# Kernel optimization log

Measured on AMD Instinct MI355X. Metric: run time of the kernel, lower is better.

The kernel has to match this reference:

```python
import jax, jax.numpy as jnp
import numpy as np

EPS = 1e-8


def setup_inputs() -> dict:
    key = jax.random.key(0)
    k1, k2, k3, k4 = jax.random.split(key, 4)
    b, cin, cout, H, W, ksz = 8, 512, 512, 64, 64, 3
    return {
        "x": jax.random.normal(k1, (b, cin, H, W), dtype=jnp.float32),
        "style": jax.random.normal(k2, (b, cin), dtype=jnp.float32),
        "noise": jax.random.normal(k3, (b, 1, H, W), dtype=jnp.float32),
        "weight": jax.random.normal(k4, (cout, cin, ksz, ksz), dtype=jnp.float32),
        "bias": jnp.zeros((1, cout, 1, 1), dtype=jnp.float32),
        "noise_strength": jnp.zeros((), dtype=jnp.float32),
    }


def reference(x, style, noise, weight, bias, noise_strength):
    cout, cin, k, _ = weight.shape
    b, _, H, W = x.shape
    scale = (1.0 / (cin * k * k)) ** 0.5

    # weight scaled and normalized by per-filter inf-norm
    w = weight * scale / jnp.max(jnp.abs(weight), axis=(1, 2, 3), keepdims=True)
    # style normalized by per-sample inf-norm
    s = style / jnp.max(jnp.abs(style), axis=1, keepdims=True)

    # modulate: (b, cout, cin, k, k)
    w = w[None] * s[:, None, :, None, None]
    # demodulate
    demod = jnp.sqrt(jnp.sum(w * w, axis=(2, 3, 4)) + EPS)  # (b, cout)
    w = w / demod[:, :, None, None, None]

    # grouped conv: one group per sample (note: input is scaled again, as in source)
    xr = (x * scale).reshape(1, b * cin, H, W)
    wr = w.reshape(b * cout, cin, k, k)
    out = jax.lax.conv_general_dilated(
        xr, wr, window_strides=(1, 1), padding=((1, 1), (1, 1)),
        dimension_numbers=("NCHW", "OIHW", "NCHW"), feature_group_count=b)
    out = out.reshape(b, cout, H, W) + bias
    out = out + noise * noise_strength
    return out
```

## Files before the change

kernel.cpp:

```cpp
#include <hip/hip_runtime.h>


#define EPSV   1e-8f
#define SCALEV 0.014731391274719738f

typedef __attribute__((ext_vector_type(8))) short short8;
typedef __attribute__((ext_vector_type(4))) float floatx4;

__device__ __forceinline__ void gload_lds16(const void* g, void* l) {
    __builtin_amdgcn_global_load_lds(
        (const __attribute__((address_space(1))) void*)g,
        (__attribute__((address_space(3))) void*)l, 16, 0, 0);
}

__device__ __forceinline__ unsigned short f2bf(float f) {
    unsigned u = __float_as_uint(f);
    unsigned r = (u + 0x7fffu + ((u >> 16) & 1u)) >> 16;
    return (unsigned short)r;
}

__global__ __launch_bounds__(256) void zero_border(uint4* __restrict__ xbp4) {
    int idx = blockIdx.x * 256 + threadIdx.x;
    if (idx >= 133120) return;
    int q    = idx & 63;
    int cell = (idx >> 6) % 260;
    int b    = idx / 16640;
    int h, w;
    if (cell < 66)       { h = 0;  w = cell; }
    else if (cell < 132) { h = 65; w = cell - 66; }
    else { int e = cell - 132; h = 1 + (e >> 1); w = (e & 1) * 65; }
    uint4 z = {0u, 0u, 0u, 0u};
    xbp4[(size_t)((b * 66 + h) * 66 + w) * 64 + q] = z;
}

__global__ __launch_bounds__(512) void prep_style(
    const float* __restrict__ style, float* __restrict__ tbuf)
{
    const int b = blockIdx.x, t = threadIdx.x;
    float v = style[b * 512 + t];
    __shared__ float red[512];
    red[t] = fabsf(v);
    __syncthreads();
    for (int s = 256; s > 0; s >>= 1) {
        if (t < s) red[t] = fmaxf(red[t], red[t + s]);
        __syncthreads();
    }
    tbuf[b * 512 + t] = v / red[0];
}

__global__ __launch_bounds__(256) void prep_w(
    const float* __restrict__ weight, float* __restrict__ wsqn,
    unsigned short* __restrict__ Aw)
{
    const int co = blockIdx.x, t = threadIdx.x;
    const float* wp = weight + (size_t)co * 4608;
    float m = 0.f;
    for (int i = t; i < 4608; i += 256) m = fmaxf(m, fabsf(wp[i]));
    __shared__ float red[256];
    red[t] = m;
    __syncthreads();
    for (int s = 128; s > 0; s >>= 1) {
        if (t < s) red[t] = fmaxf(red[t], red[t + s]);
        __syncthreads();
    }
    const float inv = 1.f / red[0];
    for (int ci = t; ci < 512; ci += 256) {
        float s = 0.f;
        #pragma unroll
        for (int k = 0; k < 9; ++k) {
            float v = wp[ci * 9 + k] * inv;
            s = fmaf(v, v, s);
            Aw[(size_t)(co * 9 + k) * 512 + ci] = f2bf(v);
        }
        wsqn[co * 512 + ci] = s;
    }
}

__global__ __launch_bounds__(256) void prep_x(
    const float* __restrict__ x, const float* __restrict__ tbuf,
    unsigned short* __restrict__ xbp)
{
    const int cic = blockIdx.x;
    const int h   = blockIdx.y;
    const int b   = blockIdx.z;
    const int tid = threadIdx.x;
    __shared__ float tr[64][33];

    const int cl = tid >> 3;
    const int w0 = (tid & 7) << 3;
    const int ci = cic * 32 + cl;
    const float tv = tbuf[b * 512 + ci];
    const float* xp = x + (((size_t)(b * 512 + ci)) << 12) + (h << 6) + w0;
    float4 u = *(const float4*)xp;
    float4 v = *(const float4*)(xp + 4);
    tr[w0 + 0][cl] = u.x * tv; tr[w0 + 1][cl] = u.y * tv;
    tr[w0 + 2][cl] = u.z * tv; tr[w0 + 3][cl] = u.w * tv;
    tr[w0 + 4][cl] = v.x * tv; tr[w0 + 5][cl] = v.y * tv;
    tr[w0 + 6][cl] = v.z * tv; tr[w0 + 7][cl] = v.w * tv;
    __syncthreads();

    const int w  = tid >> 2;
    const int c8 = (tid & 3) << 3;
    unsigned short o[8] __attribute__((aligned(16)));
    #pragma unroll
    for (int j = 0; j < 8; ++j) o[j] = f2bf(tr[w][c8 + j]);
    size_t dst = ((size_t)((b * 66 + h + 1) * 66) + (w + 1)) * 512 + cic * 32 + c8;
    *(uint4*)&xbp[dst] = *(const uint4*)o;
}

__global__ __launch_bounds__(256) void gcoef(
    const float* __restrict__ wsqn, const float* __restrict__ tbuf,
    float* __restrict__ gbuf)
{
    const int b    = blockIdx.y;
    const int co   = blockIdx.x * 4 + (threadIdx.x >> 6);
    const int lane = threadIdx.x & 63;
    float sum = 0.f;
    for (int ci = lane; ci < 512; ci += 64) {
        float tv = tbuf[b * 512 + ci];
        sum = fmaf(tv * tv, wsqn[co * 512 + ci], sum);
    }
    #pragma unroll
    for (int off = 32; off > 0; off >>= 1) sum += __shfl_down(sum, off);
    if (lane == 0)
        gbuf[b * 512 + co] = SCALEV * SCALEV / sqrtf(fmaf(SCALEV * SCALEV, sum, EPSV));
}

__global__ __launch_bounds__(256, 2) void conv_mfma(
    const unsigned short* __restrict__ xbp, const unsigned short* __restrict__ Aw,
    const float* __restrict__ gbuf, const float* __restrict__ bias,
    const float* __restrict__ noise, const float* __restrict__ nstr,
    float* __restrict__ out)
{
    __shared__ __align__(16) short sA[2][8192];
    __shared__ __align__(16) short sB[2][6656];

    const int tid  = threadIdx.x;
    const int lane = tid & 63;
    const int wv   = tid >> 6;
    const int b    = blockIdx.z;
    const int co0  = blockIdx.y << 8;
    const int h0   = (blockIdx.x >> 1) << 2;
    const int w0   = (blockIdx.x & 1) << 5;

    const int n0  = lane & 15;
    const int kq  = lane >> 4;
    const int wco = (wv >> 1) << 7;
    const int wpx = (wv & 1) << 6;

    int pb[4], aoff[8];
    #pragma unroll
    for (int fj = 0; fj < 4; ++fj) {
        int p = wpx + fj * 16 + n0;
        pb[fj] = (p >> 5) * 34 + (p & 31);
    }
    #pragma unroll
    for (int fi = 0; fi < 8; ++fi) {
        int row = wco + fi * 16 + n0;
        aoff[fi] = row * 32 + (((kq ^ (n0 >> 1)) & 3) << 3);
    }

    const int sl_px = lane >> 2;
    const int sw_ci = (((lane & 3) ^ (sl_px >> 1)) & 3) << 3;

    floatx4 zz = {0.f, 0.f, 0.f, 0.f};
    floatx4 acc[8][4];
    #pragma unroll
    for (int i = 0; i < 8; ++i)
        #pragma unroll
        for (int j = 0; j < 4; ++j) acc[i][j] = zz;

    const unsigned short* xb = xbp + (size_t)b * 4356 * 512;

    for (int ci0 = 0; ci0 < 512; ci0 += 64) {
        __syncthreads();
        #pragma unroll
        for (int hf = 0; hf < 2; ++hf) {
            const unsigned short* src = xb + ci0 + hf * 32 + sw_ci;
            for (int j = wv; j < 13; j += 4) {
                int px = j * 16 + sl_px;
                if (px > 203) px = 203;
                int row = px / 34;
                int col = px - row * 34;
                gload_lds16(src + (((size_t)(h0 + row) * 66 + w0 + col) << 9),
                            &sB[hf][j * 512]);
            }
        }
        #pragma unroll 1
        for (int pos = 0; pos < 9; ++pos) {
            const int kh = pos / 3;
            const int kw = pos - kh * 3;
            if (pos) __syncthreads();
            #pragma unroll
            for (int hf = 0; hf < 2; ++hf) {
                for (int j = wv; j < 16; j += 4) {
                    int co = j * 16 + sl_px;
                    gload_lds16(Aw + (size_t)((co0 + co) * 9 + pos) * 512
                                   + ci0 + hf * 32 + sw_ci,
                                &sA[hf][j * 512]);
                }
            }
            __syncthreads();
            const int dpos = kh * 34 + kw;
            #pragma unroll
            for (int hf = 0; hf < 2; ++hf) {
                short8 af[8], bfr[4];
                #pragma unroll
                for (int fi = 0; fi < 8; ++fi)
                    af[fi] = *(const short8*)&sA[hf][aoff[fi]];
                #pragma unroll
                for (int fj = 0; fj < 4; ++fj) {
                    int pr = pb[fj] + dpos;
                    bfr[fj] = *(const short8*)
                        &sB[hf][pr * 32 + (((kq ^ (pr >> 1)) & 3) << 3)];
                }
                #pragma unroll
                for (int fi = 0; fi < 8; ++fi)
                    #pragma unroll
                    for (int fj = 0; fj < 4; ++fj)
                        acc[fi][fj] = __builtin_amdgcn_mfma_f32_16x16x32_bf16(
                            af[fi], bfr[fj], acc[fi][fj], 0, 0, 0);
            }
        }
    }

    const float ns = nstr[0];
    float nz[4];
    int ph[4], pw[4];
    #pragma unroll
    for (int fj = 0; fj < 4; ++fj) {
        int p = wpx + fj * 16 + n0;
        ph[fj] = h0 + (p >> 5);
        pw[fj] = w0 + (p & 31);
        nz[fj] = noise[(b << 12) + (ph[fj] << 6) + pw[fj]] * ns;
    }
    #pragma unroll
    for (int fi = 0; fi < 8; ++fi) {
        #pragma unroll
        for (int i = 0; i < 4; ++i) {
            int co = co0 + wco + fi * 16 + kq * 4 + i;
            float gg = gbuf[(b << 9) + co];
            float bb = bias[co];
            #pragma unroll
            for (int fj = 0; fj < 4; ++fj) {
                out[(((size_t)((b << 9) + co)) << 12) + (ph[fj] << 6) + pw[fj]] =
                    fmaf(gg, acc[fi][fj][i], bb + nz[fj]);
            }
        }
    }
}

extern "C" void kernel_launch(void* const* d_in, const int* in_sizes, int n_in,
                              void* d_out, int out_size, void* d_ws, size_t ws_size,
                              hipStream_t stream)
{
    const float* x      = (const float*)d_in[0];
    const float* style  = (const float*)d_in[1];
    const float* noise  = (const float*)d_in[2];
    const float* weight = (const float*)d_in[3];
    const float* bias   = (const float*)d_in[4];
    const float* nstr   = (const float*)d_in[5];
    float* out = (float*)d_out;
    char* ws = (char*)d_ws;

    float*          tbuf = (float*)(ws);
    float*          gbuf = (float*)(ws + 16384);
    float*          wsqn = (float*)(ws + 32768);
    unsigned short* Aw   = (unsigned short*)(ws + 1081344);
    unsigned short* xbp  = (unsigned short*)(ws + 5799936);

    hipLaunchKernelGGL(zero_border, dim3(520), dim3(256), 0, stream, (uint4*)xbp);
    hipLaunchKernelGGL(prep_style, dim3(8), dim3(512), 0, stream, style, tbuf);
    hipLaunchKernelGGL(prep_w, dim3(512), dim3(256), 0, stream, weight, wsqn, Aw);
    hipLaunchKernelGGL(prep_x, dim3(16, 64, 8), dim3(256), 0, stream, x, tbuf, xbp);
    hipLaunchKernelGGL(gcoef, dim3(128, 8), dim3(256), 0, stream, wsqn, tbuf, gbuf);
    hipLaunchKernelGGL(conv_mfma, dim3(32, 2, 8), dim3(256), 0, stream,
                       xbp, Aw, gbuf, bias, noise, nstr, out);
}
```

Measured before the change: 272.3 us.

## Triple-buffer weight tiles in LDS to prefetch two phases ahead of MFMA

Replaces the per-position load-then-compute loop with a three-slot rotating LDS buffer for weight (A) half-tiles, issuing loads two phases ahead so global-to-LDS transfers overlap the MFMA work. Fragment reads happen before a barrier, partial vmcnt waits keep the newest prefetch in flight, and s_setprio raises priority around the MFMA block. The activation (B) tile is still reloaded synchronously at each input-channel chunk boundary. LDS use grows by one A slot, which may constrain the two-blocks-per-CU occupancy target.

Result: no change. 275.5 us (+1.2%).

```diff
diff --git a/kernel.cpp b/kernel.cpp
--- a/kernel.cpp
+++ b/kernel.cpp
@@ -132,7 +132,7 @@
     const float* __restrict__ noise, const float* __restrict__ nstr,
     float* __restrict__ out)
 {
-    __shared__ __align__(16) short sA[2][8192];
+    __shared__ __align__(16) short sA[3][8192];
     __shared__ __align__(16) short sB[2][6656];
 
     const int tid  = threadIdx.x;
@@ -172,8 +172,7 @@
 
     const unsigned short* xb = xbp + (size_t)b * 4356 * 512;
 
-    for (int ci0 = 0; ci0 < 512; ci0 += 64) {
-        __syncthreads();
+    auto stageB = [&](int ci0) {
         #pragma unroll
         for (int hf = 0; hf < 2; ++hf) {
             const unsigned short* src = xb + ci0 + hf * 32 + sw_ci;
@@ -186,53 +185,87 @@
                             &sB[hf][j * 512]);
             }
         }
+    };
+    auto stageA = [&](int ci0, int pos, int hf, int slot) {
+        for (int j = wv; j < 16; j += 4) {
+            int co = j * 16 + sl_px;
+            gload_lds16(Aw + (size_t)((co0 + co) * 9 + pos) * 512
+                           + ci0 + hf * 32 + sw_ci,
+                        &sA[slot][j * 512]);
+        }
+    };
+
+    stageB(0);
+    stageA(0, 0, 0, 0);
+    stageA(0, 0, 1, 1);
+    asm volatile("s_waitcnt vmcnt(0)" ::: "memory");
+    __builtin_amdgcn_s_barrier();
+
+    int t = 0, s = 0;
+    #pragma unroll 1
+    for (int c = 0; c < 8; ++c) {
+        const int ci0 = c << 6;
         #pragma unroll 1
-        for (int pos = 0; pos < 9; ++pos) {
-            const int kh = pos / 3;
-            const int kw = pos - kh * 3;
-            if (pos) __syncthreads();
+        for (int ph = 0; ph < 18; ++ph, ++t) {
+            const int pos  = ph >> 1;
+            const int hf   = ph & 1;
+            const int kh   = pos / 3;
+            const int dpos = kh * 34 + (pos - kh * 3);
+            const int s2   = (s >= 1) ? s - 1 : 2;
+
+            short8 af[8], bfr[4];
             #pragma unroll
-            for (int hf = 0; hf < 2; ++hf) {
-                for (int j = wv; j < 16; j += 4) {
-                    int co = j * 16 + sl_px;
-                    gload_lds16(Aw + (size_t)((co0 + co) * 9 + pos) * 512
-                                   + ci0 + hf * 32 + sw_ci,
-                                &sA[hf][j * 512]);
+            for (int fi = 0; fi < 8; ++fi)
+                af[fi] = *(const short8*)&sA[s][aoff[fi]];
+            #pragma unroll
+            for (int fj = 0; fj < 4; ++fj) {
+                int pr = pb[fj] + dpos;
+                bfr[fj] = *(const short8*)
+                    &sB[hf][pr * 32 + (((kq ^ (pr >> 1)) & 3) << 3)];
+            }
+            if (t + 2 < 144) {
+                int ph2 = ph + 2, c2 = c;
+                if (ph2 >= 18) { ph2 -= 18; ++c2; }
+                stageA(c2 << 6, ph2 >> 1, ph2 & 1, s2);
+            }
+            __builtin_amdgcn_s_barrier();
+
+            __builtin_amdgcn_s_setprio(1);
+            #pragma unroll
+            for (int fi = 0; fi < 8; ++fi)
+                #pragma unroll
+                for (int fj = 0; fj < 4; ++fj)
+                    acc[fi][fj] = __builtin_amdgcn_mfma_f32_16x16x32_bf16(
+                        af[fi], bfr[fj], acc[fi][fj], 0, 0, 0);
+            __builtin_amdgcn_s_setprio(0);
+
+            if (ph == 17) {
+                __builtin_amdgcn_s_barrier();
+                if (c < 7) {
+                    stageB(ci0 + 64);
+                    asm volatile("s_waitcnt vmcnt(0)" ::: "memory");
+                    __builtin_amdgcn_s_barrier();
                 }
-            }
-            __syncthreads();
-            const int dpos = kh * 34 + kw;
-            #pragma unroll
-            for (int hf = 0; hf < 2; ++hf) {
-                short8 af[8], bfr[4];
-                #pragma unroll
-                for (int fi = 0; fi < 8; ++fi)
-                    af[fi] = *(const short8*)&sA[hf][aoff[fi]];
-                #pragma unroll
-                for (int fj = 0; fj < 4; ++fj) {
-                    int pr = pb[fj] + dpos;
-                    bfr[fj] = *(const short8*)
-                        &sB[hf][pr * 32 + (((kq ^ (pr >> 1)) & 3) << 3)];
-                }
-                #pragma unroll
-                for (int fi = 0; fi < 8; ++fi)
-                    #pragma unroll
-                    for (int fj = 0; fj < 4; ++fj)
-                        acc[fi][fj] = __builtin_amdgcn_mfma_f32_16x16x32_bf16(
-                            af[fi], bfr[fj], acc[fi][fj], 0, 0, 0);
-            }
+            } else {
+                if (t + 2 < 144)
+                    asm volatile("s_waitcnt vmcnt(4)" ::: "memory");
+                else
+                    asm volatile("s_waitcnt vmcnt(0)" ::: "memory");
+                __builtin_amdgcn_s_barrier();
+            }
+            s = (s < 2) ? s + 1 : 0;
         }
     }
 
     const float ns = nstr[0];
     float nz[4];
-    int ph[4], pw[4];
+    int ph_[4], pw_[4];
     #pragma unroll
     for (int fj = 0; fj < 4; ++fj) {
         int p = wpx + fj * 16 + n0;
-        ph[fj] = h0 + (p >> 5);
-        pw[fj] = w0 + (p & 31);
-        nz[fj] = noise[(b << 12) + (ph[fj] << 6) + pw[fj]] * ns;
+        ph_[fj] = h0 + (p >> 5);
+        pw_[fj] = w0 + (p & 31);
+        nz[fj] = noise[(b << 12) + (ph_[fj] << 6) + pw_[fj]] * ns;
     }
     #pragma unroll
     for (int fi = 0; fi < 8; ++fi) {
@@ -243,7 +276,7 @@
             float bb = bias[co];
             #pragma unroll
             for (int fj = 0; fj < 4; ++fj) {
-                out[(((size_t)((b << 9) + co)) << 12) + (ph[fj] << 6) + pw[fj]] =
+                out[(((size_t)((b << 9) + co)) << 12) + (ph_[fj] << 6) + pw_[fj]] =
                     fmaf(gg, acc[fi][fj][i], bb + nz[fj]);
             }
         }
```

## Load weight fragments directly from global into registers, drop LDS A staging

Applied to the files above, without the earlier changes.

The weight (A) operand is no longer staged through shared memory. Each lane now loads its MFMA A fragments straight from global memory into registers, with a register double-buffer (aP/aQ) that prefetches the next half-K and position while the current MFMAs run. This removes the per-position __syncthreads pair and the A LDS traffic, and halves LDS usage. In exchange, A reads become non-shared per-wave global loads (each wave fetches its own 128 rows), which adds L2/global traffic and register pressure and may expose memory latency.

Measured after the change: 408.8 us. 1.5x slower.

```diff
diff --git a/kernel.cpp b/kernel.cpp
--- a/kernel.cpp
+++ b/kernel.cpp
@@ -132,7 +132,6 @@
     const float* __restrict__ noise, const float* __restrict__ nstr,
     float* __restrict__ out)
 {
-    __shared__ __align__(16) short sA[2][8192];
     __shared__ __align__(16) short sB[2][6656];
 
     const int tid  = threadIdx.x;
@@ -148,17 +147,15 @@
     const int wco = (wv >> 1) << 7;
     const int wpx = (wv & 1) << 6;
 
-    int pb[4], aoff[8];
+    int pb[4];
     #pragma unroll
     for (int fj = 0; fj < 4; ++fj) {
         int p = wpx + fj * 16 + n0;
         pb[fj] = (p >> 5) * 34 + (p & 31);
     }
-    #pragma unroll
-    for (int fi = 0; fi < 8; ++fi) {
-        int row = wco + fi * 16 + n0;
-        aoff[fi] = row * 32 + (((kq ^ (n0 >> 1)) & 3) << 3);
-    }
+
+    const unsigned short* Abase =
+        Aw + (size_t)(co0 + wco + n0) * 4608 + kq * 8;
 
     const int sl_px = lane >> 2;
     const int sw_ci = (((lane & 3) ^ (sl_px >> 1)) & 3) << 3;
@@ -172,8 +169,7 @@
 
     const unsigned short* xb = xbp + (size_t)b * 4356 * 512;
 
-    for (int ci0 = 0; ci0 < 512; ci0 += 64) {
-        __syncthreads();
+    auto stageB = [&](int ci0) {
         #pragma unroll
         for (int hf = 0; hf < 2; ++hf) {
             const unsigned short* src = xb + ci0 + hf * 32 + sw_ci;
@@ -186,40 +182,65 @@
                             &sB[hf][j * 512]);
             }
         }
+    };
+
+    #pragma unroll 1
+    for (int ci0 = 0; ci0 < 512; ci0 += 64) {
+        __syncthreads();
+        stageB(ci0);
+        __syncthreads();
+
+        short8 aP[8], aQ[8];
+        #pragma unroll
+        for (int fi = 0; fi < 8; ++fi)
+            aP[fi] = *(const short8*)(Abase + (size_t)fi * 73728 + ci0);
+
         #pragma unroll 1
         for (int pos = 0; pos < 9; ++pos) {
-            const int kh = pos / 3;
-            const int kw = pos - kh * 3;
-            if (pos) __syncthreads();
+            const int kh   = pos / 3;
+            const int dpos = kh * 34 + (pos - kh * 3);
+            const unsigned short* ap = Abase + pos * 512 + ci0;
+
             #pragma unroll
-            for (int hf = 0; hf < 2; ++hf) {
-                for (int j = wv; j < 16; j += 4) {
-                    int co = j * 16 + sl_px;
-                    gload_lds16(Aw + (size_t)((co0 + co) * 9 + pos) * 512
-                                   + ci0 + hf * 32 + sw_ci,
-                                &sA[hf][j * 512]);
-                }
-            }
-            __syncthreads();
-            const int dpos = kh * 34 + kw;
-            #pragma unroll
-            for (int hf = 0; hf < 2; ++hf) {
-                short8 af[8], bfr[4];
-                #pragma unroll
-                for (int fi = 0; fi < 8; ++fi)
-                    af[fi] = *(const short8*)&sA[hf][aoff[fi]];
+            for (int fi = 0; fi < 8; ++fi)
+                aQ[fi] = *(const short8*)(ap + (size_t)fi * 73728 + 32);
+
+            {
+                short8 bfr[4];
                 #pragma unroll
                 for (int fj = 0; fj < 4; ++fj) {
                     int pr = pb[fj] + dpos;
                     bfr[fj] = *(const short8*)
-                        &sB[hf][pr * 32 + (((kq ^ (pr >> 1)) & 3) << 3)];
+                        &sB[0][pr * 32 + (((kq ^ (pr >> 1)) & 3) << 3)];
                 }
                 #pragma unroll
                 for (int fi = 0; fi < 8; ++fi)
                     #pragma unroll
                     for (int fj = 0; fj < 4; ++fj)
                         acc[fi][fj] = __builtin_amdgcn_mfma_f32_16x16x32_bf16(
-                            af[fi], bfr[fj], acc[fi][fj], 0, 0, 0);
+                            aP[fi], bfr[fj], acc[fi][fj], 0, 0, 0);
+            }
+
+            if (pos < 8) {
+                #pragma unroll
+                for (int fi = 0; fi < 8; ++fi)
+                    aP[fi] = *(const short8*)(ap + (size_t)fi * 73728 + 512);
+            }
+
+            {
+                short8 bfr[4];
+                #pragma unroll
+                for (int fj = 0; fj < 4; ++fj) {
+                    int pr = pb[fj] + dpos;
+                    bfr[fj] = *(const short8*)
+                        &sB[1][pr * 32 + (((kq ^ (pr >> 1)) & 3) << 3)];
+                }
+                #pragma unroll
+                for (int fi = 0; fi < 8; ++fi)
+                    #pragma unroll
+                    for (int fj = 0; fj < 4; ++fj)
+                        acc[fi][fj] = __builtin_amdgcn_mfma_f32_16x16x32_bf16(
+                            aQ[fi], bfr[fj], acc[fi][fj], 0, 0, 0);
             }
         }
     }
```
